# Kernel tuning notes

Measured on AMD Instinct MI355X. Metric: run time of the kernel, lower is better.

## Reference

```python
import jax, jax.numpy as jnp
import numpy as np

IN_C, OUT_C, K, STRIDE, PAD = 128, 256, 3, 1, 1


def setup_inputs() -> dict:
    key = jax.random.key(0)
    kx, kw = jax.random.split(key)
    x = jax.random.normal(kx, (32, IN_C, 56, 56), dtype=jnp.float32)
    weight = jax.random.normal(kw, (OUT_C, IN_C, K, K), dtype=jnp.float32) * 0.02
    bias = jnp.zeros((OUT_C,), dtype=jnp.float32)
    return {"x": x, "weight": weight, "bias": bias}


def reference(x, weight, bias):
    # Faithful conv2d: zero-pad + im2col + GEMM in the torch module is
    # mathematically a standard cross-correlation conv; use the fused primitive.
    out = jax.lax.conv_general_dilated(
        x, weight,
        window_strides=(STRIDE, STRIDE),
        padding=[(PAD, PAD), (PAD, PAD)],
        dimension_numbers=("NCHW", "OIHW", "NCHW"),
    )
    out = out + bias[None, :, None, None]
    return out
```

## Files before the change

### kernel.cpp

```cpp
#include <hip/hip_runtime.h>


typedef __attribute__((ext_vector_type(8))) short short8;
typedef __attribute__((ext_vector_type(4))) float f32x4;

#define HWSZ 56
#define HW2 3136
#define INC 128
#define OUTC 256
#define NBATCH 32
#define NPIX (NBATCH * HW2)
#define KTOT 1152
#define XT_ELEMS 12845056

__device__ __forceinline__ unsigned short f2b(float f) {
    union { float f; unsigned u; } v; v.f = f;
    unsigned r = v.u + 0x7fffu + ((v.u >> 16) & 1u);
    return (unsigned short)(r >> 16);
}

__global__ __launch_bounds__(256) void xt_kernel(const float* __restrict__ x,
                                                 unsigned short* __restrict__ xt) {
    __shared__ float tile[128][65];
    const int b = blockIdx.x;
    const int n = b / 49;
    const int hw0 = (b - n * 49) * 64;
    const int t = threadIdx.x;

    const float* xp = x + (size_t)n * (INC * HW2) + hw0;
    const int c_base = t >> 4;
    const int hwo = (t & 15) * 4;
#pragma unroll
    for (int j = 0; j < 8; ++j) {
        const int c = j * 16 + c_base;
        const f32x4 v = *reinterpret_cast<const f32x4*>(xp + c * HW2 + hwo);
        tile[c][hwo + 0] = v[0];
        tile[c][hwo + 1] = v[1];
        tile[c][hwo + 2] = v[2];
        tile[c][hwo + 3] = v[3];
    }
    __syncthreads();
    const int hw = t >> 2;
    const int c0 = (t & 3) * 32;
    unsigned short* dst = xt + ((size_t)(n * HW2 + hw0 + hw)) * INC + c0;
#pragma unroll
    for (int g = 0; g < 4; ++g) {
        short8 v;
#pragma unroll
        for (int e = 0; e < 8; ++e) v[e] = (short)f2b(tile[c0 + g * 8 + e][hw]);
        reinterpret_cast<short8*>(dst)[g] = v;
    }
}

__global__ __launch_bounds__(256) void wt_kernel(const float* __restrict__ w,
                                                 unsigned short* __restrict__ wt) {
    const int tid = blockIdx.x * 256 + threadIdx.x;
    const int oc = tid / KTOT;
    const int r = tid - oc * KTOT;
    const int pos = r >> 7;
    const int ic = r & 127;
    wt[tid] = f2b(w[oc * KTOT + ic * 9 + pos]);
}

__global__ __launch_bounds__(256, 2) void conv_main(const unsigned short* __restrict__ xt,
                                                    const unsigned short* __restrict__ wt,
                                                    const float* __restrict__ bias,
                                                    float* __restrict__ out) {
    __shared__ unsigned short As[128][40];
    __shared__ unsigned short Bs[128][40];

    const int bid = blockIdx.x;
    const int work = (bid & 7) * 196 + (bid >> 3);
    const int oc0 = (work & 1) * 128;
    const int P0 = (work >> 1) * 128;

    const int t = threadIdx.x;
    const int lane = t & 63;
    const int wid = t >> 6;
    const int wr = wid >> 1;
    const int wc = wid & 1;
    const int fr = lane & 15;
    const int fq = lane >> 4;

    const int srow = t >> 1;
    const int scol = (t & 1) * 16;
    const unsigned short* wt_base = wt + (oc0 + srow) * KTOT + scol;

    const int P = P0 + srow;
    const int n = P / HW2;
    const int hw = P - n * HW2;
    const int oh = hw / HWSZ;
    const int ow = hw - oh * HWSZ;
    const unsigned short* xt_img = xt + (size_t)n * (HW2 * INC);

    f32x4 acc[4][4];
#pragma unroll
    for (int i = 0; i < 4; ++i)
#pragma unroll
        for (int j = 0; j < 4; ++j) {
            f32x4 z = {0.f, 0.f, 0.f, 0.f};
            acc[i][j] = z;
        }

    const short8 zero8 = {0, 0, 0, 0, 0, 0, 0, 0};
    short8 ra0, ra1, rb0, rb1;

    auto load_tiles = [&](int s, short8& a0, short8& a1, short8& b0, short8& b1) {
        const int pos = s >> 2;
        const int icc = s & 3;
        const short8* ap = reinterpret_cast<const short8*>(wt_base + pos * 128 + icc * 32);
        a0 = ap[0];
        a1 = ap[1];
        const int kh = pos / 3;
        const int kw = pos - kh * 3;
        const int ih = oh + kh - 1;
        const int iw = ow + kw - 1;
        if ((unsigned)ih < (unsigned)HWSZ && (unsigned)iw < (unsigned)HWSZ) {
            const short8* bp = reinterpret_cast<const short8*>(
                xt_img + (ih * HWSZ + iw) * INC + icc * 32 + scol);
            b0 = bp[0];
            b1 = bp[1];
        } else {
            b0 = zero8;
            b1 = zero8;
        }
    };

    load_tiles(0, ra0, ra1, rb0, rb1);

    for (int s = 0; s < 36; ++s) {
        __syncthreads();
        *reinterpret_cast<short8*>(&As[srow][scol]) = ra0;
        *reinterpret_cast<short8*>(&As[srow][scol + 8]) = ra1;
        *reinterpret_cast<short8*>(&Bs[srow][scol]) = rb0;
        *reinterpret_cast<short8*>(&Bs[srow][scol + 8]) = rb1;
        __syncthreads();
        if (s < 35) load_tiles(s + 1, ra0, ra1, rb0, rb1);

        short8 af[4], bf[4];
#pragma unroll
        for (int mi = 0; mi < 4; ++mi)
            af[mi] = *reinterpret_cast<const short8*>(&As[wr * 64 + mi * 16 + fr][fq * 8]);
#pragma unroll
        for (int ni = 0; ni < 4; ++ni)
            bf[ni] = *reinterpret_cast<const short8*>(&Bs[wc * 64 + ni * 16 + fr][fq * 8]);
#pragma unroll
        for (int mi = 0; mi < 4; ++mi)
#pragma unroll
            for (int ni = 0; ni < 4; ++ni)
                acc[mi][ni] = __builtin_amdgcn_mfma_f32_16x16x32_bf16(af[mi], bf[ni],
                                                                      acc[mi][ni], 0, 0, 0);
    }

    float bmr[4][4];
#pragma unroll
    for (int mi = 0; mi < 4; ++mi)
#pragma unroll
        for (int r = 0; r < 4; ++r)
            bmr[mi][r] = bias[oc0 + wr * 64 + mi * 16 + fq * 4 + r];

#pragma unroll
    for (int ni = 0; ni < 4; ++ni) {
        const int Pp = P0 + wc * 64 + ni * 16 + fr;
        const int nn = Pp / HW2;
        const int hwp = Pp - nn * HW2;
        float* op = out + (size_t)nn * (OUTC * HW2) + hwp;
#pragma unroll
        for (int mi = 0; mi < 4; ++mi)
#pragma unroll
            for (int r = 0; r < 4; ++r) {
                const int oc = oc0 + wr * 64 + mi * 16 + fq * 4 + r;
                op[oc * HW2] = acc[mi][ni][r] + bmr[mi][r];
            }
    }
}

extern "C" void kernel_launch(void* const* d_in, const int* in_sizes, int n_in,
                              void* d_out, int out_size, void* d_ws, size_t ws_size,
                              hipStream_t stream) {
    const float* x = (const float*)d_in[0];
    const float* w = (const float*)d_in[1];
    const float* bias = (const float*)d_in[2];
    float* out = (float*)d_out;

    unsigned short* xt = (unsigned short*)d_ws;
    unsigned short* wt = xt + XT_ELEMS;

    xt_kernel<<<1568, 256, 0, stream>>>(x, xt);
    wt_kernel<<<1152, 256, 0, stream>>>(w, wt);
    conv_main<<<1568, 256, 0, stream>>>(xt, wt, bias, out);
}
```

Before: 220.1 us.

## Use padded NHWC input, pre-swizzled weights, and direct global-to-LDS double buffering

The input transpose now writes into a zero-padded 58x58 NHWC buffer, cleared with a memset, so the conv loop needs no boundary checks. Weights are pre-packed into per-stage swizzled 128x32 panels. The main loop loads A and B tiles straight into a double-buffered LDS using global_load_lds, with an XOR swizzle to avoid bank conflicts. This removes the register staging and one barrier per step, but adds a memset of the padded buffer and more LDS.

```diff
diff --git a/kernel.cpp b/kernel.cpp
--- a/kernel.cpp
+++ b/kernel.cpp
@@ -3,24 +3,31 @@
 
 typedef __attribute__((ext_vector_type(8))) short short8;
 typedef __attribute__((ext_vector_type(4))) float f32x4;
+typedef unsigned short ushort_t;
 
 #define HWSZ 56
 #define HW2 3136
 #define INC 128
 #define OUTC 256
-#define NBATCH 32
-#define NPIX (NBATCH * HW2)
-#define KTOT 1152
-#define XT_ELEMS 12845056
-
-__device__ __forceinline__ unsigned short f2b(float f) {
+#define NPIX 100352
+#define PADW 58
+#define XT_ELEMS 13778944
+#define XT_BYTES 27557888
+
+__device__ __forceinline__ ushort_t f2b(float f) {
     union { float f; unsigned u; } v; v.f = f;
     unsigned r = v.u + 0x7fffu + ((v.u >> 16) & 1u);
-    return (unsigned short)(r >> 16);
+    return (ushort_t)(r >> 16);
+}
+
+__device__ __forceinline__ void glds16(const void* g, void* l) {
+    __builtin_amdgcn_global_load_lds(
+        (const __attribute__((address_space(1))) unsigned*)g,
+        (__attribute__((address_space(3))) unsigned*)l, 16, 0, 0);
 }
 
 __global__ __launch_bounds__(256) void xt_kernel(const float* __restrict__ x,
-                                                 unsigned short* __restrict__ xt) {
+                                                 ushort_t* __restrict__ xt) {
     __shared__ float tile[128][65];
     const int b = blockIdx.x;
     const int n = b / 49;
@@ -41,117 +48,120 @@
     }
     __syncthreads();
     const int hw = t >> 2;
-    const int c0 = (t & 3) * 32;
-    unsigned short* dst = xt + ((size_t)(n * HW2 + hw0 + hw)) * INC + c0;
+    const int q = t & 3;
+    const int P = hw0 + hw;
+    const int oh = P / HWSZ;
+    const int ow = P - oh * HWSZ;
+    ushort_t* dst = xt + (((size_t)n * PADW + oh + 1) * PADW + (ow + 1)) * INC;
 #pragma unroll
     for (int g = 0; g < 4; ++g) {
         short8 v;
 #pragma unroll
-        for (int e = 0; e < 8; ++e) v[e] = (short)f2b(tile[c0 + g * 8 + e][hw]);
-        reinterpret_cast<short8*>(dst)[g] = v;
+        for (int e = 0; e < 8; ++e) v[e] = (short)f2b(tile[g * 32 + q * 8 + e][hw]);
+        *reinterpret_cast<short8*>(dst + g * 32 + q * 8) = v;
     }
 }
 
 __global__ __launch_bounds__(256) void wt_kernel(const float* __restrict__ w,
-                                                 unsigned short* __restrict__ wt) {
+                                                 ushort_t* __restrict__ wt2) {
     const int tid = blockIdx.x * 256 + threadIdx.x;
-    const int oc = tid / KTOT;
-    const int r = tid - oc * KTOT;
-    const int pos = r >> 7;
-    const int ic = r & 127;
-    wt[tid] = f2b(w[oc * KTOT + ic * 9 + pos]);
-}
-
-__global__ __launch_bounds__(256, 2) void conv_main(const unsigned short* __restrict__ xt,
-                                                    const unsigned short* __restrict__ wt,
+    const int panel = tid >> 9;
+    const int s = tid & 511;
+    const int oc_tile = panel / 36;
+    const int rem = panel - oc_tile * 36;
+    const int pos = rem >> 2;
+    const int icc = rem & 3;
+    const int row = s >> 2;
+    const int fq = (s & 3) ^ ((row >> 1) & 3);
+    const int oc = oc_tile * 128 + row;
+    const int ic0 = icc * 32 + fq * 8;
+    short8 v;
+#pragma unroll
+    for (int e = 0; e < 8; ++e) v[e] = (short)f2b(w[(oc * 128 + ic0 + e) * 9 + pos]);
+    *reinterpret_cast<short8*>(wt2 + (size_t)tid * 8) = v;
+}
+
+__global__ __launch_bounds__(256, 2) void conv_main(const ushort_t* __restrict__ xt,
+                                                    const ushort_t* __restrict__ wt2,
                                                     const float* __restrict__ bias,
                                                     float* __restrict__ out) {
-    __shared__ unsigned short As[128][40];
-    __shared__ unsigned short Bs[128][40];
+    __shared__ ushort_t lds[2][2][4096];
 
     const int bid = blockIdx.x;
     const int work = (bid & 7) * 196 + (bid >> 3);
-    const int oc0 = (work & 1) * 128;
+    const int oc_tile = work & 1;
     const int P0 = (work >> 1) * 128;
 
     const int t = threadIdx.x;
-    const int lane = t & 63;
-    const int wid = t >> 6;
-    const int wr = wid >> 1;
-    const int wc = wid & 1;
-    const int fr = lane & 15;
-    const int fq = lane >> 4;
-
-    const int srow = t >> 1;
-    const int scol = (t & 1) * 16;
-    const unsigned short* wt_base = wt + (oc0 + srow) * KTOT + scol;
-
-    const int P = P0 + srow;
-    const int n = P / HW2;
-    const int hw = P - n * HW2;
-    const int oh = hw / HWSZ;
-    const int ow = hw - oh * HWSZ;
-    const unsigned short* xt_img = xt + (size_t)n * (HW2 * INC);
+    const int w = t >> 6;
+    const int l = t & 63;
+    const int fr = l & 15;
+    const int fq = l >> 4;
+    const int wr = w >> 1;
+    const int wc = w & 1;
+
+    const ushort_t* Abase = wt2 + (size_t)oc_tile * (36 * 4096) + t * 8;
+
+    const int pa = w * 16 + (l >> 2);
+    const int Pa = P0 + pa;
+    const int na = Pa / HW2; const int hwa = Pa - na * HW2;
+    const int oha = hwa / HWSZ; const int owa = hwa - oha * HWSZ;
+    const int Pb = Pa + 64;
+    const int nb = Pb / HW2; const int hwb = Pb - nb * HW2;
+    const int ohb = hwb / HWSZ; const int owb = hwb - ohb * HWSZ;
+    const ushort_t* xra = xt + (((size_t)na * PADW + oha) * PADW + owa) * INC;
+    const ushort_t* xrb = xt + (((size_t)nb * PADW + ohb) * PADW + owb) * INC;
+    const int swz = ((l & 3) ^ ((l >> 3) & 3)) * 8;
+
+    const int frag_off = fr * 32 + ((fq ^ ((fr >> 1) & 3)) * 8);
 
     f32x4 acc[4][4];
 #pragma unroll
     for (int i = 0; i < 4; ++i)
 #pragma unroll
-        for (int j = 0; j < 4; ++j) {
-            f32x4 z = {0.f, 0.f, 0.f, 0.f};
-            acc[i][j] = z;
+        for (int j = 0; j < 4; ++j) { f32x4 z = {0.f,0.f,0.f,0.f}; acc[i][j] = z; }
+
+    glds16(Abase,            &lds[0][0][w * 512]);
+    glds16(Abase + 2048,     &lds[0][0][(w + 4) * 512]);
+    glds16(xra + swz,        &lds[0][1][w * 512]);
+    glds16(xrb + swz,        &lds[0][1][(w + 4) * 512]);
+    __syncthreads();
+
+    int cur = 0;
+    for (int s = 0; s < 36; ++s) {
+        if (s < 35) {
+            const int s1 = s + 1;
+            const int pos = s1 >> 2;
+            const int icc = s1 & 3;
+            const int kh = pos / 3;
+            const int kw = pos - kh * 3;
+            const int koff = (kh * PADW + kw) * INC + icc * 32;
+            const ushort_t* Ab = Abase + s1 * 4096;
+            glds16(Ab,               &lds[cur ^ 1][0][w * 512]);
+            glds16(Ab + 2048,        &lds[cur ^ 1][0][(w + 4) * 512]);
+            glds16(xra + koff + swz, &lds[cur ^ 1][1][w * 512]);
+            glds16(xrb + koff + swz, &lds[cur ^ 1][1][(w + 4) * 512]);
         }
-
-    const short8 zero8 = {0, 0, 0, 0, 0, 0, 0, 0};
-    short8 ra0, ra1, rb0, rb1;
-
-    auto load_tiles = [&](int s, short8& a0, short8& a1, short8& b0, short8& b1) {
-        const int pos = s >> 2;
-        const int icc = s & 3;
-        const short8* ap = reinterpret_cast<const short8*>(wt_base + pos * 128 + icc * 32);
-        a0 = ap[0];
-        a1 = ap[1];
-        const int kh = pos / 3;
-        const int kw = pos - kh * 3;
-        const int ih = oh + kh - 1;
-        const int iw = ow + kw - 1;
-        if ((unsigned)ih < (unsigned)HWSZ && (unsigned)iw < (unsigned)HWSZ) {
-            const short8* bp = reinterpret_cast<const short8*>(
-                xt_img + (ih * HWSZ + iw) * INC + icc * 32 + scol);
-            b0 = bp[0];
-            b1 = bp[1];
-        } else {
-            b0 = zero8;
-            b1 = zero8;
-        }
-    };
-
-    load_tiles(0, ra0, ra1, rb0, rb1);
-
-    for (int s = 0; s < 36; ++s) {
-        __syncthreads();
-        *reinterpret_cast<short8*>(&As[srow][scol]) = ra0;
-        *reinterpret_cast<short8*>(&As[srow][scol + 8]) = ra1;
-        *reinterpret_cast<short8*>(&Bs[srow][scol]) = rb0;
-        *reinterpret_cast<short8*>(&Bs[srow][scol + 8]) = rb1;
-        __syncthreads();
-        if (s < 35) load_tiles(s + 1, ra0, ra1, rb0, rb1);
-
+        const ushort_t* A = &lds[cur][0][0];
+        const ushort_t* B = &lds[cur][1][0];
         short8 af[4], bf[4];
 #pragma unroll
         for (int mi = 0; mi < 4; ++mi)
-            af[mi] = *reinterpret_cast<const short8*>(&As[wr * 64 + mi * 16 + fr][fq * 8]);
+            af[mi] = *reinterpret_cast<const short8*>(A + wr * 2048 + mi * 512 + frag_off);
 #pragma unroll
         for (int ni = 0; ni < 4; ++ni)
-            bf[ni] = *reinterpret_cast<const short8*>(&Bs[wc * 64 + ni * 16 + fr][fq * 8]);
+            bf[ni] = *reinterpret_cast<const short8*>(B + wc * 2048 + ni * 512 + frag_off);
 #pragma unroll
         for (int mi = 0; mi < 4; ++mi)
 #pragma unroll
             for (int ni = 0; ni < 4; ++ni)
                 acc[mi][ni] = __builtin_amdgcn_mfma_f32_16x16x32_bf16(af[mi], bf[ni],
                                                                       acc[mi][ni], 0, 0, 0);
-    }
-
+        __syncthreads();
+        cur ^= 1;
+    }
+
+    const int oc0 = oc_tile * 128;
     float bmr[4][4];
 #pragma unroll
     for (int mi = 0; mi < 4; ++mi)
@@ -183,10 +193,11 @@
     const float* bias = (const float*)d_in[2];
     float* out = (float*)d_out;
 
-    unsigned short* xt = (unsigned short*)d_ws;
-    unsigned short* wt = xt + XT_ELEMS;
-
+    ushort_t* xt = (ushort_t*)d_ws;
+    ushort_t* wt2 = xt + XT_ELEMS;
+
+    hipMemsetAsync(d_ws, 0, XT_BYTES, stream);
     xt_kernel<<<1568, 256, 0, stream>>>(x, xt);
-    wt_kernel<<<1152, 256, 0, stream>>>(w, wt);
-    conv_main<<<1568, 256, 0, stream>>>(xt, wt, bias, out);
-}
+    wt_kernel<<<144, 256, 0, stream>>>(w, wt2);
+    conv_main<<<1568, 256, 0, stream>>>(xt, wt2, bias, out);
+}
```

New measurement: 204.3 us. 1.08x faster.
